# Kernel optimization log

Measured on AMD Instinct MI355X. Metric: run time of the kernel, lower is better.

Reference implementation:

```python
import jax, jax.numpy as jnp
import numpy as np
from jax import lax

B, S, T = 1024, 1024, 20


def setup_inputs() -> dict:
    key = jax.random.key(0)
    k1, k2, k3, k4 = jax.random.split(key, 4)
    return {
        "emissions": jax.random.normal(k1, (B, S, T), dtype=jnp.float32),
        "start_transitions": jax.random.normal(k2, (T,), dtype=jnp.float32) * 0.1,
        "end_transitions": jax.random.normal(k3, (T,), dtype=jnp.float32) * 0.1,
        "transitions": jax.random.normal(k4, (T, T), dtype=jnp.float32) * 0.1,
    }


def reference(emissions, start_transitions, end_transitions, transitions):
    # Viterbi decode, all-ones mask (torchcrf.CRF.decode with batch_first=True).
    # emissions: [B, S, T] -> best tag sequence [B, S] (int32)
    em = jnp.swapaxes(emissions, 0, 1)  # [S, B, T]
    score0 = start_transitions[None, :] + em[0]  # [B, T]

    def fwd_step(score, emit):
        # score[b, i] + transitions[i, j] -> [B, T_i, T_j]
        cand = score[:, :, None] + transitions[None, :, :]
        best = jnp.max(cand, axis=1) + emit  # [B, T]
        bp = jnp.argmax(cand, axis=1).astype(jnp.int32)  # [B, T]
        return best, bp

    final_score, bps = lax.scan(fwd_step, score0, em[1:])  # bps: [S-1, B, T]
    final_score = final_score + end_transitions[None, :]
    last_tag = jnp.argmax(final_score, axis=1).astype(jnp.int32)  # [B]

    def back_step(tag, bp):
        # tag: best tag at step s; bp[b, j] = best prev tag given tag j at s
        prev = jnp.take_along_axis(bp, tag[:, None], axis=1)[:, 0]
        return prev, tag

    first_tag, tags_rest = lax.scan(back_step, last_tag, bps, reverse=True)
    # tags_rest: [S-1, B] tags for positions 1..S-1; first_tag: [B] position 0
    all_tags = jnp.concatenate([first_tag[None, :], tags_rest], axis=0)  # [S, B]
    return jnp.swapaxes(all_tags, 0, 1)  # [B, S]
```

## Files before the change

kernel.cpp:

```cpp
#include <hip/hip_runtime.h>
#include <stdint.h>

#define BB 1024
#define SS 1024
#define TT 20

#define L2 16
#define C2 (SS / L2)

#define MERGE(vd, id, va, ia, vb, ib)  \
    {                                  \
        bool ge = (va) >= (vb);        \
        vd = ge ? (va) : (vb);         \
        id = ge ? (ia) : (ib);         \
    }

#define RL(x, i) __uint_as_float(__builtin_amdgcn_readlane(__float_as_uint(x), i))

__device__ __forceinline__ void argmax20(
    float c0, float c1, float c2, float c3, float c4, float c5, float c6,
    float c7, float c8, float c9, float c10, float c11, float c12, float c13,
    float c14, float c15, float c16, float c17, float c18, float c19,
    float& best, int& bidx)
{
    float m0, m1, m2, m3, m4, m5, m6, m7, m8, m9;
    int i0, i1, i2, i3, i4, i5, i6, i7, i8, i9;
    MERGE(m0, i0, c0, 0, c1, 1);
    MERGE(m1, i1, c2, 2, c3, 3);
    MERGE(m2, i2, c4, 4, c5, 5);
    MERGE(m3, i3, c6, 6, c7, 7);
    MERGE(m4, i4, c8, 8, c9, 9);
    MERGE(m5, i5, c10, 10, c11, 11);
    MERGE(m6, i6, c12, 12, c13, 13);
    MERGE(m7, i7, c14, 14, c15, 15);
    MERGE(m8, i8, c16, 16, c17, 17);
    MERGE(m9, i9, c18, 18, c19, 19);

    float n0, n1, n2, n3, n4;
    int j0, j1, j2, j3, j4;
    MERGE(n0, j0, m0, i0, m1, i1);
    MERGE(n1, j1, m2, i2, m3, i3);
    MERGE(n2, j2, m4, i4, m5, i5);
    MERGE(n3, j3, m6, i6, m7, i7);
    MERGE(n4, j4, m8, i8, m9, i9);

    float p0, p1;
    int k0, k1;
    MERGE(p0, k0, n0, j0, n1, j1);
    MERGE(p1, k1, n2, j2, n3, j3);

    float q0;
    int l0;
    MERGE(q0, l0, p0, k0, p1, k1);

    MERGE(best, bidx, q0, l0, n4, j4);
}

__global__ __launch_bounds__(64) void fwd_kernel(
    const float* __restrict__ em,
    const float* __restrict__ startt,
    const float* __restrict__ endt,
    const float* __restrict__ trans,
    uint8_t* __restrict__ bp,
    int* __restrict__ last_tag)
{
    const int b = blockIdx.x;
    const int lane = threadIdx.x;
    const int p = (lane < 20) ? 0 : ((lane < 40) ? 1 : 2);
    const int jr = lane - 20 * p;
    const int j = (jr < TT) ? jr : (TT - 1);
    const int ibase = 7 * p;

    const int i0 = ibase,     i1 = ibase + 1, i2 = ibase + 2, i3 = ibase + 3;
    const int i4 = ibase + 4, i5 = ibase + 5;
    const int i6 = (ibase + 6 > TT - 1) ? (TT - 1) : (ibase + 6);

    const float tr0 = trans[i0 * TT + j], tr1 = trans[i1 * TT + j];
    const float tr2 = trans[i2 * TT + j], tr3 = trans[i3 * TT + j];
    const float tr4 = trans[i4 * TT + j], tr5 = trans[i5 * TT + j];
    const float tr6 = trans[i6 * TT + j];

    const float* emb = em + (size_t)b * SS * TT;
    float score = startt[j] + emb[j];

    uint8_t* bpb = bp + (size_t)b * TT + lane;

    const int l20 = (lane + 20) & 63;
    const int l40 = (lane + 40) & 63;

    float f0 = emb[(size_t)1 * TT + j],  f1 = emb[(size_t)2 * TT + j];
    float f2 = emb[(size_t)3 * TT + j],  f3 = emb[(size_t)4 * TT + j];
    float f4 = emb[(size_t)5 * TT + j],  f5 = emb[(size_t)6 * TT + j];
    float f6 = emb[(size_t)7 * TT + j],  f7 = emb[(size_t)8 * TT + j];
    float f8 = emb[(size_t)9 * TT + j],  f9 = emb[(size_t)10 * TT + j];
    float f10 = emb[(size_t)11 * TT + j], f11 = emb[(size_t)12 * TT + j];
    float f12 = emb[(size_t)13 * TT + j], f13 = emb[(size_t)14 * TT + j];
    float f14 = emb[(size_t)15 * TT + j], f15 = emb[(size_t)16 * TT + j];

#define VSTEP_CORE(scur, FREG)                                              \
    {                                                                       \
        const float ecur = FREG;                                            \
        const float s0 = __shfl(score, i0, 64);                             \
        const float s1 = __shfl(score, i1, 64);                             \
        const float s2 = __shfl(score, i2, 64);                             \
        const float s3 = __shfl(score, i3, 64);                             \
        const float s4 = __shfl(score, i4, 64);                             \
        const float s5 = __shfl(score, i5, 64);                             \
        const float s6 = __shfl(score, i6, 64);                             \
        const float c0 = s0 + tr0, c1 = s1 + tr1, c2 = s2 + tr2;            \
        const float c3 = s3 + tr3, c4 = s4 + tr4, c5 = s5 + tr5;            \
        const float c6 = s6 + tr6;                                          \
        float a0, a1, a2, b0v, b1v, rv;                                     \
        int x0, x1, x2, y0, y1, xr;                                         \
        MERGE(a0, x0, c0, i0, c1, i1);                                      \
        MERGE(a1, x1, c2, i2, c3, i3);                                      \
        MERGE(a2, x2, c4, i4, c5, i5);                                      \
        MERGE(b0v, y0, a0, x0, a1, x1);                                     \
        MERGE(b1v, y1, a2, x2, c6, i6);                                     \
        MERGE(rv, xr, b0v, y0, b1v, y1);                                    \
        const float g1v = __shfl(rv, l20, 64);                              \
        const int   g1x = __shfl(xr, l20, 64);                              \
        const float g2v = __shfl(rv, l40, 64);                              \
        const int   g2x = __shfl(xr, l40, 64);                              \
        float m01, mf;                                                      \
        int z01, zf;                                                        \
        MERGE(m01, z01, rv, xr, g1v, g1x);                                  \
        MERGE(mf, zf, m01, z01, g2v, g2x);                                  \
        score = mf + ecur;                                                  \
        if (lane < TT) bpb[(size_t)(scur) * (BB * TT)] = (uint8_t)zf;       \
    }

#define VSTEP(scur, FREG)                                                   \
    {                                                                       \
        VSTEP_CORE(scur, FREG);                                             \
        const int sn_ = (scur) + 16;                                        \
        const int snc_ = sn_ > (SS - 1) ? (SS - 1) : sn_;                   \
        FREG = emb[(size_t)snc_ * TT + j];                                  \
    }

    for (int s = 1; s <= SS - 31; s += 16) {
        VSTEP(s + 0, f0);
        VSTEP(s + 1, f1);
        VSTEP(s + 2, f2);
        VSTEP(s + 3, f3);
        VSTEP(s + 4, f4);
        VSTEP(s + 5, f5);
        VSTEP(s + 6, f6);
        VSTEP(s + 7, f7);
        VSTEP(s + 8, f8);
        VSTEP(s + 9, f9);
        VSTEP(s + 10, f10);
        VSTEP(s + 11, f11);
        VSTEP(s + 12, f12);
        VSTEP(s + 13, f13);
        VSTEP(s + 14, f14);
        VSTEP(s + 15, f15);
    }

    VSTEP_CORE(SS - 15, f0);
    VSTEP_CORE(SS - 14, f1);
    VSTEP_CORE(SS - 13, f2);
    VSTEP_CORE(SS - 12, f3);
    VSTEP_CORE(SS - 11, f4);
    VSTEP_CORE(SS - 10, f5);
    VSTEP_CORE(SS - 9, f6);
    VSTEP_CORE(SS - 8, f7);
    VSTEP_CORE(SS - 7, f8);
    VSTEP_CORE(SS - 6, f9);
    VSTEP_CORE(SS - 5, f10);
    VSTEP_CORE(SS - 4, f11);
    VSTEP_CORE(SS - 3, f12);
    VSTEP_CORE(SS - 2, f13);
    VSTEP_CORE(SS - 1, f14);

    const float fin = score + endt[j];
    {
        const float g0 = RL(fin, 0), g1 = RL(fin, 1), g2 = RL(fin, 2);
        const float g3 = RL(fin, 3), g4 = RL(fin, 4), g5 = RL(fin, 5);
        const float g6 = RL(fin, 6), g7 = RL(fin, 7), g8 = RL(fin, 8);
        const float g9 = RL(fin, 9), g10 = RL(fin, 10), g11 = RL(fin, 11);
        const float g12 = RL(fin, 12), g13 = RL(fin, 13), g14 = RL(fin, 14);
        const float g15 = RL(fin, 15), g16 = RL(fin, 16), g17 = RL(fin, 17);
        const float g18 = RL(fin, 18), g19 = RL(fin, 19);
        float best;
        int bidx;
        argmax20(g0, g1, g2, g3, g4, g5, g6, g7, g8, g9, g10, g11, g12, g13,
                 g14, g15, g16, g17, g18, g19, best, bidx);
        if (lane == 0) last_tag[b] = bidx;
    }
}

__global__ void bt_compose(const uint8_t* __restrict__ bp, uint8_t* __restrict__ G)
{
    const int tid = blockIdx.x * blockDim.x + threadIdx.x;
    const int total = BB * (C2 - 1) * TT;
    if (tid >= total) return;
    const int j = tid % TT;
    const int r = tid / TT;
    const int c = 1 + (r % (C2 - 1));
    const int b = r / (C2 - 1);

    int t = j;
    const int hi = (c + 1) * L2 - 1;
#pragma unroll
    for (int k = 0; k < L2; ++k) {
        const int s = hi - k;
        t = bp[((size_t)s * BB + b) * TT + t];
    }
    G[((size_t)c * BB + b) * TT + j] = (uint8_t)t;
}

__global__ void bt_scan(const uint8_t* __restrict__ G,
                        const int* __restrict__ last_tag,
                        int* __restrict__ xtag)
{
    const int b = blockIdx.x * blockDim.x + threadIdx.x;
    if (b >= BB) return;
    int x = last_tag[b];
    xtag[(size_t)(C2 - 1) * BB + b] = x;
    for (int c = C2 - 1; c >= 1; --c) {
        x = G[((size_t)c * BB + b) * TT + x];
        xtag[(size_t)(c - 1) * BB + b] = x;
    }
}

__global__ void bt_expand(const uint8_t* __restrict__ bp,
                          const int* __restrict__ xtag,
                          int* __restrict__ out)
{
    const int tid = blockIdx.x * blockDim.x + threadIdx.x;
    if (tid >= BB * C2) return;
    const int c = tid % C2;
    const int b = tid / C2;

    int t = xtag[(size_t)c * BB + b];
    const int hi = (c + 1) * L2 - 1;
    int* ob = out + (size_t)b * SS;
    ob[hi] = t;
#pragma unroll
    for (int k = 0; k < L2 - 1; ++k) {
        const int s = hi - k;
        t = bp[((size_t)s * BB + b) * TT + t];
        ob[s - 1] = t;
    }
}

extern "C" void kernel_launch(void* const* d_in, const int* in_sizes, int n_in,
                              void* d_out, int out_size, void* d_ws, size_t ws_size,
                              hipStream_t stream) {
    const float* em = (const float*)d_in[0];
    const float* st = (const float*)d_in[1];
    const float* en = (const float*)d_in[2];
    const float* tr = (const float*)d_in[3];
    int* out = (int*)d_out;

    const size_t SBT = (size_t)SS * BB * TT;
    uint8_t* bp = (uint8_t*)d_ws;
    int* last_tag = (int*)((char*)d_ws + SBT);
    uint8_t* G = (uint8_t*)d_ws + SBT + 4096;
    int* xtag = (int*)((char*)d_ws + SBT + 4096 + (size_t)C2 * BB * TT);

    fwd_kernel<<<BB, 64, 0, stream>>>(em, st, en, tr, bp, last_tag);

    const int tot1 = BB * (C2 - 1) * TT;
    bt_compose<<<(tot1 + 255) / 256, 256, 0, stream>>>(bp, G);
    bt_scan<<<(BB + 255) / 256, 256, 0, stream>>>(G, last_tag, xtag);
    bt_expand<<<(BB * C2 + 255) / 256, 256, 0, stream>>>(bp, xtag, out);
}
```

Baseline: 275.0 us.

## Split predecessor max across wave halves with permlane32 swap and equality-mask argmax

Reorganizes the per-step Viterbi max so each half of the wavefront handles 10 predecessor states instead of three 20-lane groups handling 7 each. The two halves are combined with a single permlane32 swap rather than four cross-lane shuffles. The argmax is recovered afterwards by comparing candidates to the final max and taking the lowest matching index, which removes the index-carrying select chain from the critical path. The cost is more broadcast shuffles per step (10 instead of 7), and tie-breaking now picks the lowest index, which may differ from the old ordering.

```diff
diff --git a/kernel.cpp b/kernel.cpp
--- a/kernel.cpp
+++ b/kernel.cpp
@@ -7,6 +7,26 @@
 
 #define L2 16
 #define C2 (SS / L2)
+
+typedef unsigned uvec2 __attribute__((ext_vector_type(2)));
+
+__device__ __forceinline__ float swap_half_f(float x, bool lowhalf) {
+#if __has_builtin(__builtin_amdgcn_permlane32_swap)
+    uvec2 r = __builtin_amdgcn_permlane32_swap(__float_as_uint(x),
+                                               __float_as_uint(x), false, false);
+    return __uint_as_float(lowhalf ? r.y : r.x);
+#else
+    return __shfl(x, (int)(threadIdx.x ^ 32), 64);
+#endif
+}
+__device__ __forceinline__ int swap_half_i(int x, bool lowhalf) {
+#if __has_builtin(__builtin_amdgcn_permlane32_swap)
+    uvec2 r = __builtin_amdgcn_permlane32_swap((unsigned)x, (unsigned)x, false, false);
+    return (int)(lowhalf ? r.y : r.x);
+#else
+    return __shfl(x, (int)(threadIdx.x ^ 32), 64);
+#endif
+}
 
 #define MERGE(vd, id, va, ia, vb, ib)  \
     {                                  \
@@ -66,27 +86,26 @@
 {
     const int b = blockIdx.x;
     const int lane = threadIdx.x;
-    const int p = (lane < 20) ? 0 : ((lane < 40) ? 1 : 2);
-    const int jr = lane - 20 * p;
+    const bool lowhalf = lane < 32;
+    const int jr = lowhalf ? lane : (lane - 32);
     const int j = (jr < TT) ? jr : (TT - 1);
-    const int ibase = 7 * p;
-
-    const int i0 = ibase,     i1 = ibase + 1, i2 = ibase + 2, i3 = ibase + 3;
-    const int i4 = ibase + 4, i5 = ibase + 5;
-    const int i6 = (ibase + 6 > TT - 1) ? (TT - 1) : (ibase + 6);
-
-    const float tr0 = trans[i0 * TT + j], tr1 = trans[i1 * TT + j];
-    const float tr2 = trans[i2 * TT + j], tr3 = trans[i3 * TT + j];
-    const float tr4 = trans[i4 * TT + j], tr5 = trans[i5 * TT + j];
-    const float tr6 = trans[i6 * TT + j];
+    const int rbase = lowhalf ? 0 : 10;
+
+    const float tr0 = trans[(rbase + 0) * TT + j];
+    const float tr1 = trans[(rbase + 1) * TT + j];
+    const float tr2 = trans[(rbase + 2) * TT + j];
+    const float tr3 = trans[(rbase + 3) * TT + j];
+    const float tr4 = trans[(rbase + 4) * TT + j];
+    const float tr5 = trans[(rbase + 5) * TT + j];
+    const float tr6 = trans[(rbase + 6) * TT + j];
+    const float tr7 = trans[(rbase + 7) * TT + j];
+    const float tr8 = trans[(rbase + 8) * TT + j];
+    const float tr9 = trans[(rbase + 9) * TT + j];
 
     const float* emb = em + (size_t)b * SS * TT;
     float score = startt[j] + emb[j];
 
     uint8_t* bpb = bp + (size_t)b * TT + lane;
-
-    const int l20 = (lane + 20) & 63;
-    const int l40 = (lane + 40) & 63;
 
     float f0 = emb[(size_t)1 * TT + j],  f1 = emb[(size_t)2 * TT + j];
     float f2 = emb[(size_t)3 * TT + j],  f3 = emb[(size_t)4 * TT + j];
@@ -100,33 +119,37 @@
 #define VSTEP_CORE(scur, FREG)                                              \
     {                                                                       \
         const float ecur = FREG;                                            \
-        const float s0 = __shfl(score, i0, 64);                             \
-        const float s1 = __shfl(score, i1, 64);                             \
-        const float s2 = __shfl(score, i2, 64);                             \
-        const float s3 = __shfl(score, i3, 64);                             \
-        const float s4 = __shfl(score, i4, 64);                             \
-        const float s5 = __shfl(score, i5, 64);                             \
-        const float s6 = __shfl(score, i6, 64);                             \
+        const float s0 = __shfl(score, rbase + 0, 64);                      \
+        const float s1 = __shfl(score, rbase + 1, 64);                      \
+        const float s2 = __shfl(score, rbase + 2, 64);                      \
+        const float s3 = __shfl(score, rbase + 3, 64);                      \
+        const float s4 = __shfl(score, rbase + 4, 64);                      \
+        const float s5 = __shfl(score, rbase + 5, 64);                      \
+        const float s6 = __shfl(score, rbase + 6, 64);                      \
+        const float s7 = __shfl(score, rbase + 7, 64);                      \
+        const float s8 = __shfl(score, rbase + 8, 64);                      \
+        const float s9 = __shfl(score, rbase + 9, 64);                      \
         const float c0 = s0 + tr0, c1 = s1 + tr1, c2 = s2 + tr2;            \
         const float c3 = s3 + tr3, c4 = s4 + tr4, c5 = s5 + tr5;            \
-        const float c6 = s6 + tr6;                                          \
-        float a0, a1, a2, b0v, b1v, rv;                                     \
-        int x0, x1, x2, y0, y1, xr;                                         \
-        MERGE(a0, x0, c0, i0, c1, i1);                                      \
-        MERGE(a1, x1, c2, i2, c3, i3);                                      \
-        MERGE(a2, x2, c4, i4, c5, i5);                                      \
-        MERGE(b0v, y0, a0, x0, a1, x1);                                     \
-        MERGE(b1v, y1, a2, x2, c6, i6);                                     \
-        MERGE(rv, xr, b0v, y0, b1v, y1);                                    \
-        const float g1v = __shfl(rv, l20, 64);                              \
-        const int   g1x = __shfl(xr, l20, 64);                              \
-        const float g2v = __shfl(rv, l40, 64);                              \
-        const int   g2x = __shfl(xr, l40, 64);                              \
-        float m01, mf;                                                      \
-        int z01, zf;                                                        \
-        MERGE(m01, z01, rv, xr, g1v, g1x);                                  \
-        MERGE(mf, zf, m01, z01, g2v, g2x);                                  \
+        const float c6 = s6 + tr6, c7 = s7 + tr7, c8 = s8 + tr8;            \
+        const float c9 = s9 + tr9;                                          \
+                       \
+        const float v0 = fmaxf(fmaxf(c0, c1), c2);                          \
+        const float v1 = fmaxf(fmaxf(c3, c4), c5);                          \
+        const float v2 = fmaxf(fmaxf(c6, c7), c8);                          \
+        const float rv = fmaxf(fmaxf(fmaxf(v0, v1), v2), c9);               \
+        const float crossv = swap_half_f(rv, lowhalf);                      \
+        const float mf = fmaxf(rv, crossv);                                 \
         score = mf + ecur;                                                  \
+            \
+        unsigned msk = ((c0 == mf) ? 1u : 0u) | ((c1 == mf) ? 2u : 0u) |    \
+                       ((c2 == mf) ? 4u : 0u) | ((c3 == mf) ? 8u : 0u) |    \
+                       ((c4 == mf) ? 16u : 0u) | ((c5 == mf) ? 32u : 0u) |  \
+                       ((c6 == mf) ? 64u : 0u) | ((c7 == mf) ? 128u : 0u) | \
+                       ((c8 == mf) ? 256u : 0u) | ((c9 == mf) ? 512u : 0u); \
+        const int fm = rbase + __builtin_ctz(msk | 0x80000000u);            \
+        const int fmx = swap_half_i(fm, lowhalf);                           \
+        const int zf = (fm < fmx) ? fm : fmx;                               \
         if (lane < TT) bpb[(size_t)(scur) * (BB * TT)] = (uint8_t)zf;       \
     }
 
```

After: 313.2 us. +13.9%, slower.

## Replace lane-split shuffle argmax with readlane broadcast and max-then-match index

Applied to the files above, without the earlier changes.

The Viterbi forward step no longer splits the 20 source tags across three lane groups that exchange partial results through shuffles. Each of lanes 0–19 now receives all 20 previous scores through scalar readlane broadcasts and keeps all 20 transition values in registers. The max is a fmax tree, and the argmax index is found afterwards by comparing each candidate against the max, with ties resolved to the lowest index. This removes the cross-lane shuffle round trips (LDS/permute latency) from the serial dependency chain. In exchange each lane does more arithmetic, lanes 20–63 sit idle, and the twenty v_readlane operations may serialise through the scalar unit.

```diff
diff --git a/kernel.cpp b/kernel.cpp
--- a/kernel.cpp
+++ b/kernel.cpp
@@ -7,6 +7,8 @@
 
 #define L2 16
 #define C2 (SS / L2)
+
+#define RL(x, i) __uint_as_float(__builtin_amdgcn_readlane(__float_as_uint(x), i))
 
 #define MERGE(vd, id, va, ia, vb, ib)  \
     {                                  \
@@ -14,8 +16,6 @@
         vd = ge ? (va) : (vb);         \
         id = ge ? (ia) : (ib);         \
     }
-
-#define RL(x, i) __uint_as_float(__builtin_amdgcn_readlane(__float_as_uint(x), i))
 
 __device__ __forceinline__ void argmax20(
     float c0, float c1, float c2, float c3, float c4, float c5, float c6,
@@ -66,27 +66,23 @@
 {
     const int b = blockIdx.x;
     const int lane = threadIdx.x;
-    const int p = (lane < 20) ? 0 : ((lane < 40) ? 1 : 2);
-    const int jr = lane - 20 * p;
-    const int j = (jr < TT) ? jr : (TT - 1);
-    const int ibase = 7 * p;
-
-    const int i0 = ibase,     i1 = ibase + 1, i2 = ibase + 2, i3 = ibase + 3;
-    const int i4 = ibase + 4, i5 = ibase + 5;
-    const int i6 = (ibase + 6 > TT - 1) ? (TT - 1) : (ibase + 6);
-
-    const float tr0 = trans[i0 * TT + j], tr1 = trans[i1 * TT + j];
-    const float tr2 = trans[i2 * TT + j], tr3 = trans[i3 * TT + j];
-    const float tr4 = trans[i4 * TT + j], tr5 = trans[i5 * TT + j];
-    const float tr6 = trans[i6 * TT + j];
+    const int j = (lane < TT) ? lane : (TT - 1);
+
+    const float t0 = trans[0 * TT + j],  t1 = trans[1 * TT + j];
+    const float t2 = trans[2 * TT + j],  t3 = trans[3 * TT + j];
+    const float t4 = trans[4 * TT + j],  t5 = trans[5 * TT + j];
+    const float t6 = trans[6 * TT + j],  t7 = trans[7 * TT + j];
+    const float t8 = trans[8 * TT + j],  t9 = trans[9 * TT + j];
+    const float t10 = trans[10 * TT + j], t11 = trans[11 * TT + j];
+    const float t12 = trans[12 * TT + j], t13 = trans[13 * TT + j];
+    const float t14 = trans[14 * TT + j], t15 = trans[15 * TT + j];
+    const float t16 = trans[16 * TT + j], t17 = trans[17 * TT + j];
+    const float t18 = trans[18 * TT + j], t19 = trans[19 * TT + j];
 
     const float* emb = em + (size_t)b * SS * TT;
     float score = startt[j] + emb[j];
 
     uint8_t* bpb = bp + (size_t)b * TT + lane;
-
-    const int l20 = (lane + 20) & 63;
-    const int l40 = (lane + 40) & 63;
 
     float f0 = emb[(size_t)1 * TT + j],  f1 = emb[(size_t)2 * TT + j];
     float f2 = emb[(size_t)3 * TT + j],  f3 = emb[(size_t)4 * TT + j];
@@ -100,33 +96,60 @@
 #define VSTEP_CORE(scur, FREG)                                              \
     {                                                                       \
         const float ecur = FREG;                                            \
-        const float s0 = __shfl(score, i0, 64);                             \
-        const float s1 = __shfl(score, i1, 64);                             \
-        const float s2 = __shfl(score, i2, 64);                             \
-        const float s3 = __shfl(score, i3, 64);                             \
-        const float s4 = __shfl(score, i4, 64);                             \
-        const float s5 = __shfl(score, i5, 64);                             \
-        const float s6 = __shfl(score, i6, 64);                             \
-        const float c0 = s0 + tr0, c1 = s1 + tr1, c2 = s2 + tr2;            \
-        const float c3 = s3 + tr3, c4 = s4 + tr4, c5 = s5 + tr5;            \
-        const float c6 = s6 + tr6;                                          \
-        float a0, a1, a2, b0v, b1v, rv;                                     \
-        int x0, x1, x2, y0, y1, xr;                                         \
-        MERGE(a0, x0, c0, i0, c1, i1);                                      \
-        MERGE(a1, x1, c2, i2, c3, i3);                                      \
-        MERGE(a2, x2, c4, i4, c5, i5);                                      \
-        MERGE(b0v, y0, a0, x0, a1, x1);                                     \
-        MERGE(b1v, y1, a2, x2, c6, i6);                                     \
-        MERGE(rv, xr, b0v, y0, b1v, y1);                                    \
-        const float g1v = __shfl(rv, l20, 64);                              \
-        const int   g1x = __shfl(xr, l20, 64);                              \
-        const float g2v = __shfl(rv, l40, 64);                              \
-        const int   g2x = __shfl(xr, l40, 64);                              \
-        float m01, mf;                                                      \
-        int z01, zf;                                                        \
-        MERGE(m01, z01, rv, xr, g1v, g1x);                                  \
-        MERGE(mf, zf, m01, z01, g2v, g2x);                                  \
+              \
+        const float c0 = RL(score, 0) + t0;                                 \
+        const float c1 = RL(score, 1) + t1;                                 \
+        const float c2 = RL(score, 2) + t2;                                 \
+        const float c3 = RL(score, 3) + t3;                                 \
+        const float c4 = RL(score, 4) + t4;                                 \
+        const float c5 = RL(score, 5) + t5;                                 \
+        const float c6 = RL(score, 6) + t6;                                 \
+        const float c7 = RL(score, 7) + t7;                                 \
+        const float c8 = RL(score, 8) + t8;                                 \
+        const float c9 = RL(score, 9) + t9;                                 \
+        const float c10 = RL(score, 10) + t10;                              \
+        const float c11 = RL(score, 11) + t11;                              \
+        const float c12 = RL(score, 12) + t12;                              \
+        const float c13 = RL(score, 13) + t13;                              \
+        const float c14 = RL(score, 14) + t14;                              \
+        const float c15 = RL(score, 15) + t15;                              \
+        const float c16 = RL(score, 16) + t16;                              \
+        const float c17 = RL(score, 17) + t17;                              \
+        const float c18 = RL(score, 18) + t18;                              \
+        const float c19 = RL(score, 19) + t19;                              \
+                     \
+        const float x0 = fmaxf(fmaxf(c0, c1), c2);                          \
+        const float x1 = fmaxf(fmaxf(c3, c4), c5);                          \
+        const float x2 = fmaxf(fmaxf(c6, c7), c8);                          \
+        const float x3 = fmaxf(fmaxf(c9, c10), c11);                        \
+        const float x4 = fmaxf(fmaxf(c12, c13), c14);                       \
+        const float x5 = fmaxf(fmaxf(c15, c16), c17);                       \
+        const float x6 = fmaxf(c18, c19);                                   \
+        const float y0 = fmaxf(fmaxf(x0, x1), x2);                          \
+        const float y1 = fmaxf(fmaxf(x3, x4), x5);                          \
+        const float mf = fmaxf(fmaxf(y0, y1), x6);                          \
         score = mf + ecur;                                                  \
+         \
+        int zf = 19;                                                        \
+        zf = (c18 == mf) ? 18 : zf;                                         \
+        zf = (c17 == mf) ? 17 : zf;                                         \
+        zf = (c16 == mf) ? 16 : zf;                                         \
+        zf = (c15 == mf) ? 15 : zf;                                         \
+        zf = (c14 == mf) ? 14 : zf;                                         \
+        zf = (c13 == mf) ? 13 : zf;                                         \
+        zf = (c12 == mf) ? 12 : zf;                                         \
+        zf = (c11 == mf) ? 11 : zf;                                         \
+        zf = (c10 == mf) ? 10 : zf;                                         \
+        zf = (c9 == mf) ? 9 : zf;                                           \
+        zf = (c8 == mf) ? 8 : zf;                                           \
+        zf = (c7 == mf) ? 7 : zf;                                           \
+        zf = (c6 == mf) ? 6 : zf;                                           \
+        zf = (c5 == mf) ? 5 : zf;                                           \
+        zf = (c4 == mf) ? 4 : zf;                                           \
+        zf = (c3 == mf) ? 3 : zf;                                           \
+        zf = (c2 == mf) ? 2 : zf;                                           \
+        zf = (c1 == mf) ? 1 : zf;                                           \
+        zf = (c0 == mf) ? 0 : zf;                                           \
         if (lane < TT) bpb[(size_t)(scur) * (BB * TT)] = (uint8_t)zf;       \
     }
 
```

Measured after the change: 391.6 us. 1.42x slower.

## Split value max from argmax recovery in Viterbi step to shorten the dependency chain

Applied to the files above, without the earlier changes.

Each Viterbi step now reduces only the max value, using fmaxf within each lane group plus two value shuffles across groups. It no longer carries index pairs through every merge and shuffle. The argmax index is recovered afterwards by comparing each candidate to the final max, and the lowest-index group holding the max writes the backpointer, which preserves first-index tie-breaking. Score shuffles now read from lanes in the thread's own group rather than from lanes 0-19. The aim is to cut shuffles and selects on the serial per-step critical path, at the cost of extra equality compares and a divergent store.

```diff
diff --git a/kernel.cpp b/kernel.cpp
--- a/kernel.cpp
+++ b/kernel.cpp
@@ -7,6 +7,8 @@
 
 #define L2 16
 #define C2 (SS / L2)
+
+#define RL(x, i) __uint_as_float(__builtin_amdgcn_readlane(__float_as_uint(x), i))
 
 #define MERGE(vd, id, va, ia, vb, ib)  \
     {                                  \
@@ -14,8 +16,6 @@
         vd = ge ? (va) : (vb);         \
         id = ge ? (ia) : (ib);         \
     }
-
-#define RL(x, i) __uint_as_float(__builtin_amdgcn_readlane(__float_as_uint(x), i))
 
 __device__ __forceinline__ void argmax20(
     float c0, float c1, float c2, float c3, float c4, float c5, float c6,
@@ -66,27 +66,37 @@
 {
     const int b = blockIdx.x;
     const int lane = threadIdx.x;
-    const int p = (lane < 20) ? 0 : ((lane < 40) ? 1 : 2);
+    const int p = (lane < 20) ? 0 : (lane < 40) ? 1 : 2;
     const int jr = lane - 20 * p;
     const int j = (jr < TT) ? jr : (TT - 1);
-    const int ibase = 7 * p;
-
-    const int i0 = ibase,     i1 = ibase + 1, i2 = ibase + 2, i3 = ibase + 3;
-    const int i4 = ibase + 4, i5 = ibase + 5;
-    const int i6 = (ibase + 6 > TT - 1) ? (TT - 1) : (ibase + 6);
-
-    const float tr0 = trans[i0 * TT + j], tr1 = trans[i1 * TT + j];
-    const float tr2 = trans[i2 * TT + j], tr3 = trans[i3 * TT + j];
-    const float tr4 = trans[i4 * TT + j], tr5 = trans[i5 * TT + j];
-    const float tr6 = trans[i6 * TT + j];
+    const bool isp0 = (p == 0);
+    const bool isp1 = (p == 1);
+    const bool isp2 = (p == 2);
+    const int rb = 7 * p;
+    const int r6c = (rb + 6 > TT - 1) ? (TT - 1) : (rb + 6);
+
+    const float tr0 = trans[(rb + 0) * TT + j];
+    const float tr1 = trans[(rb + 1) * TT + j];
+    const float tr2 = trans[(rb + 2) * TT + j];
+    const float tr3 = trans[(rb + 3) * TT + j];
+    const float tr4 = trans[(rb + 4) * TT + j];
+    const float tr5 = trans[(rb + 5) * TT + j];
+    const float tr6 = trans[r6c * TT + j];
+
+    const int sl0 = 20 * p + rb + 0;
+    const int sl1 = 20 * p + rb + 1;
+    const int sl2 = 20 * p + rb + 2;
+    const int sl3 = 20 * p + rb + 3;
+    const int sl4 = 20 * p + rb + 4;
+    const int sl5 = 20 * p + rb + 5;
+    const int sl6 = 20 * p + r6c;
+    const int la = 20 * ((p + 1) % 3) + j;
+    const int lb = 20 * ((p + 2) % 3) + j;
 
     const float* emb = em + (size_t)b * SS * TT;
     float score = startt[j] + emb[j];
 
-    uint8_t* bpb = bp + (size_t)b * TT + lane;
-
-    const int l20 = (lane + 20) & 63;
-    const int l40 = (lane + 40) & 63;
+    uint8_t* bpcol = bp + (size_t)b * TT + j;
 
     float f0 = emb[(size_t)1 * TT + j],  f1 = emb[(size_t)2 * TT + j];
     float f2 = emb[(size_t)3 * TT + j],  f3 = emb[(size_t)4 * TT + j];
@@ -100,34 +110,41 @@
 #define VSTEP_CORE(scur, FREG)                                              \
     {                                                                       \
         const float ecur = FREG;                                            \
-        const float s0 = __shfl(score, i0, 64);                             \
-        const float s1 = __shfl(score, i1, 64);                             \
-        const float s2 = __shfl(score, i2, 64);                             \
-        const float s3 = __shfl(score, i3, 64);                             \
-        const float s4 = __shfl(score, i4, 64);                             \
-        const float s5 = __shfl(score, i5, 64);                             \
-        const float s6 = __shfl(score, i6, 64);                             \
+                   \
+        const float s0 = __shfl(score, sl0, 64);                            \
+        const float s1 = __shfl(score, sl1, 64);                            \
+        const float s2 = __shfl(score, sl2, 64);                            \
+        const float s3 = __shfl(score, sl3, 64);                            \
+        const float s4 = __shfl(score, sl4, 64);                            \
+        const float s5 = __shfl(score, sl5, 64);                            \
+        const float s6 = __shfl(score, sl6, 64);                            \
         const float c0 = s0 + tr0, c1 = s1 + tr1, c2 = s2 + tr2;            \
         const float c3 = s3 + tr3, c4 = s4 + tr4, c5 = s5 + tr5;            \
         const float c6 = s6 + tr6;                                          \
-        float a0, a1, a2, b0v, b1v, rv;                                     \
-        int x0, x1, x2, y0, y1, xr;                                         \
-        MERGE(a0, x0, c0, i0, c1, i1);                                      \
-        MERGE(a1, x1, c2, i2, c3, i3);                                      \
-        MERGE(a2, x2, c4, i4, c5, i5);                                      \
-        MERGE(b0v, y0, a0, x0, a1, x1);                                     \
-        MERGE(b1v, y1, a2, x2, c6, i6);                                     \
-        MERGE(rv, xr, b0v, y0, b1v, y1);                                    \
-        const float g1v = __shfl(rv, l20, 64);                              \
-        const int   g1x = __shfl(xr, l20, 64);                              \
-        const float g2v = __shfl(rv, l40, 64);                              \
-        const int   g2x = __shfl(xr, l40, 64);                              \
-        float m01, mf;                                                      \
-        int z01, zf;                                                        \
-        MERGE(m01, z01, rv, xr, g1v, g1x);                                  \
-        MERGE(mf, zf, m01, z01, g2v, g2x);                                  \
+                                             \
+        const float t01 = fmaxf(c0, c1);                                    \
+        const float t23 = fmaxf(c2, c3);                                    \
+        const float t45 = fmaxf(c4, c5);                                    \
+        const float u0 = fmaxf(t01, t23);                                   \
+        const float u1 = fmaxf(t45, c6);                                    \
+        const float rv = fmaxf(u0, u1);                                     \
+                                     \
+        const float rva = __shfl(rv, la, 64);                               \
+        const float rvb = __shfl(rv, lb, 64);                               \
+        const float mf = fmaxf(fmaxf(rv, rva), rvb);                        \
         score = mf + ecur;                                                  \
-        if (lane < TT) bpb[(size_t)(scur) * (BB * TT)] = (uint8_t)zf;       \
+         \
+        int fm = r6c;                                                       \
+        fm = (c5 == mf) ? rb + 5 : fm;                                      \
+        fm = (c4 == mf) ? rb + 4 : fm;                                      \
+        fm = (c3 == mf) ? rb + 3 : fm;                                      \
+        fm = (c2 == mf) ? rb + 2 : fm;                                      \
+        fm = (c1 == mf) ? rb + 1 : fm;                                      \
+        fm = (c0 == mf) ? rb + 0 : fm;                                      \
+        const float e0v = isp1 ? rvb : rva;   \
+        const bool win = (rv == mf) && (isp0 || e0v != mf) &&               \
+                         (!isp2 || rvb != mf);                              \
+        if (win && jr < TT) bpcol[(size_t)(scur) * (BB * TT)] = (uint8_t)fm; \
     }
 
 #define VSTEP(scur, FREG)                                                   \
```

After: 283.9 us. 1.03x slower.
